# Kernel tuning notes

Hardware: AMD Instinct MI355X
Metric: run time of the kernel (lower is better)

The kernel has to match this reference:

```python
import jax, jax.numpy as jnp
import numpy as np

NUM_GROUPS = 32
EPS = 1e-6


def group_norm(x, gamma, beta):
    # x: (b, c, h, w) -> normalize within 32 groups over (c/g, h, w)
    b, c, h, w = x.shape
    g = NUM_GROUPS
    xg = x.reshape(b, g, c // g, h, w)
    mean = xg.mean(axis=(2, 3, 4), keepdims=True)
    var = xg.var(axis=(2, 3, 4), keepdims=True)
    xg = (xg - mean) * jax.lax.rsqrt(var + EPS)
    xn = xg.reshape(b, c, h, w)
    return xn * gamma[None, :, None, None] + beta[None, :, None, None]


def setup_inputs() -> dict:
    key = jax.random.key(0)
    ks = jax.random.split(key, 4)
    b, c, h, w = 4, 512, 64, 64
    x = jax.random.normal(ks[0], (b, c, h, w), dtype=jnp.float32)
    gamma = jnp.ones((c,), dtype=jnp.float32)
    beta = jnp.zeros((c,), dtype=jnp.float32)
    w_qkv = jax.random.normal(ks[1], (3 * c, c), dtype=jnp.float32) * (1.0 / np.sqrt(c))
    b_qkv = jnp.zeros((3 * c,), dtype=jnp.float32)
    # NOTE: original init zeroes proj weight; use small random weights so the
    # attention path contributes to output/gradients in the baseline.
    w_proj = jax.random.normal(ks[2], (c, c), dtype=jnp.float32) * 0.02
    b_proj = jnp.zeros((c,), dtype=jnp.float32)
    return {"x": x, "gamma": gamma, "beta": beta, "w_qkv": w_qkv,
            "b_qkv": b_qkv, "w_proj": w_proj, "b_proj": b_proj}


def reference(x, gamma, beta, w_qkv, b_qkv, w_proj, b_proj):
    b, c, h, w = x.shape
    scale = c ** (-0.25)
    identity = x
    xn = group_norm(x, gamma, beta)
    # 1x1 conv == channel matmul: (b,c,h,w) x (3c,c) -> (b,3c,h,w)
    qkv = jnp.einsum('bchw,oc->bohw', xn, w_qkv) + b_qkv[None, :, None, None]
    qkv = qkv.reshape(b, 3 * c, h * w)
    q, k, v = jnp.split(qkv, 3, axis=1)          # each (b, c, N)
    attn = jnp.einsum('bci,bcj->bij', q * scale, k * scale)  # (b, N, N)
    attn = jax.nn.softmax(attn, axis=-1)
    out = jnp.einsum('bij,bcj->bci', attn, v)    # (b, c, N)
    out = out.reshape(b, c, h, w)
    out = jnp.einsum('bchw,oc->bohw', out, w_proj) + b_proj[None, :, None, None]
    return out + identity
```

## Files before the change

kernel.cpp:

```cpp
#include <hip/hip_runtime.h>
#include <hip/hip_fp8.h>
#include <stdint.h>

typedef unsigned short u16;
typedef unsigned char u8;
typedef __bf16 bf16x8 __attribute__((ext_vector_type(8)));
typedef float f32x4 __attribute__((ext_vector_type(4)));

__device__ __forceinline__ u16 f2bf(float f) {
  union { float f; unsigned u; } v; v.f = f;
  return (u16)((v.u + 0x7FFFu + ((v.u >> 16) & 1u)) >> 16);
}
__device__ __forceinline__ u8 f2f8(float f) {
  __hip_fp8_e4m3 h(f);
  return (u8)h.__x;
}

__device__ __forceinline__ void gld_lds16(const void* g, void* l) {
  uint32_t lo = (uint32_t)(uintptr_t)l;
  lo = __builtin_amdgcn_readfirstlane(lo);
  auto* lp = (__attribute__((address_space(3))) uint32_t*)(uintptr_t)lo;
  auto* gp = (const __attribute__((address_space(1))) uint32_t*)(uintptr_t)g;
  __builtin_amdgcn_global_load_lds(gp, lp, 16, 0, 0);
}

__device__ __forceinline__ void bar() {
  __builtin_amdgcn_sched_barrier(0);
  __builtin_amdgcn_s_barrier();
  __builtin_amdgcn_sched_barrier(0);
}

__global__ __launch_bounds__(256) void cvt_weights(
    const float* __restrict__ wq, const float* __restrict__ wp,
    u16* __restrict__ oq, u16* __restrict__ op) {
  int i = blockIdx.x * 256 + threadIdx.x;
  if (i < 1536 * 512) oq[i] = f2bf(wq[i]);
  if (i < 512 * 512)  op[i] = f2bf(wp[i]);
}

__global__ __launch_bounds__(256) void gn_stats(const float* __restrict__ x,
                                                float* __restrict__ stats) {
  int bg = blockIdx.x;
  const float* p = x + (size_t)bg * 65536;
  float s = 0.f, sq = 0.f;
  for (int i = threadIdx.x * 4; i < 65536; i += 1024) {
    float4 v = *(const float4*)(p + i);
    s += v.x + v.y + v.z + v.w;
    sq += v.x * v.x + v.y * v.y + v.z * v.z + v.w * v.w;
  }
  int lane = threadIdx.x & 63, w = threadIdx.x >> 6;
  for (int off = 32; off; off >>= 1) {
    s += __shfl_down(s, off);
    sq += __shfl_down(sq, off);
  }
  __shared__ float ls[4], lq[4];
  if (lane == 0) { ls[w] = s; lq[w] = sq; }
  __syncthreads();
  if (threadIdx.x == 0) {
    float S = ls[0] + ls[1] + ls[2] + ls[3];
    float Q = lq[0] + lq[1] + lq[2] + lq[3];
    float mean = S * (1.f / 65536.f);
    float var = Q * (1.f / 65536.f) - mean * mean;
    stats[bg * 2] = mean;
    stats[bg * 2 + 1] = rsqrtf(var + 1e-6f);
  }
}

__global__ __launch_bounds__(256) void gn_norm_t(const float* __restrict__ x,
    const float* __restrict__ stats, const float* __restrict__ gamma,
    const float* __restrict__ beta, u16* __restrict__ xnT) {
  __shared__ u16 tile[64][72];
  int b = blockIdx.z;
  int c0 = blockIdx.y * 64, n0 = blockIdx.x * 64;
  int t = threadIdx.x;
  int cl = t >> 2, ng = (t & 3) * 16;
  int c = c0 + cl;
  float mean = stats[(b * 32 + (c >> 4)) * 2];
  float rstd = stats[(b * 32 + (c >> 4)) * 2 + 1];
  float a = gamma[c] * rstd;
  float b2 = beta[c] - mean * a;
  const float* src = x + ((size_t)b * 512 + c) * 4096 + n0 + ng;
  u16 e[16];
  #pragma unroll
  for (int q = 0; q < 4; ++q) {
    float4 v = *(const float4*)(src + q * 4);
    e[q * 4 + 0] = f2bf(v.x * a + b2);
    e[q * 4 + 1] = f2bf(v.y * a + b2);
    e[q * 4 + 2] = f2bf(v.z * a + b2);
    e[q * 4 + 3] = f2bf(v.w * a + b2);
  }
  #pragma unroll
  for (int j = 0; j < 16; ++j) tile[ng + j][cl] = e[j];
  __syncthreads();
  int nl = t >> 2, cg = (t & 3) * 16;
  uint4 w0 = *(const uint4*)&tile[nl][cg];
  uint4 w1 = *(const uint4*)&tile[nl][cg + 8];
  u16* dst = xnT + ((size_t)b * 4096 + n0 + nl) * 512 + c0 + cg;
  *(uint4*)dst = w0;
  *(uint4*)(dst + 8) = w1;
}

template<int EPI>
__global__ __launch_bounds__(256) void gemm_nt(
    const u16* __restrict__ A, const u16* __restrict__ B,
    int lda, int ldb, int K,
    const float* __restrict__ bias, const float* __restrict__ resid,
    float scale, float* __restrict__ outF, void* __restrict__ outBv, int ldo,
    size_t azs, size_t bzs, size_t ozs) {
  __shared__ __align__(16) u16 smem[16384];
  const size_t z = blockIdx.z;
  A += z * azs; B += z * bzs;
  const int t = threadIdx.x;
  const int wave = t >> 6, lane = t & 63;
  const int wm = wave >> 1, wn = wave & 1;
  const int quad = lane >> 4, li = lane & 15;
  const int m0 = blockIdx.y * 128, n0 = blockIdx.x * 128;

  const int srow = lane >> 2;
  const int scol = (lane & 3) * 8;
  const u16* gA[2];
  const u16* gB[2];
  int ldsOff[2];
  #pragma unroll
  for (int r = 0; r < 2; ++r) {
    int rb = wave + 4 * r;
    gA[r] = A + (size_t)(m0 + rb * 16 + srow) * lda + scol;
    gB[r] = B + (size_t)(n0 + rb * 16 + srow) * ldb + scol;
    ldsOff[r] = rb * 512;
  }

  f32x4 zero = {0.f, 0.f, 0.f, 0.f};
  f32x4 acc[4][4];
  #pragma unroll
  for (int i = 0; i < 4; ++i)
    #pragma unroll
    for (int j = 0; j < 4; ++j) acc[i][j] = zero;

  #pragma unroll
  for (int r = 0; r < 2; ++r) {
    gld_lds16(gA[r], &smem[ldsOff[r]]);
    gld_lds16(gB[r], &smem[8192 + ldsOff[r]]);
  }
  __syncthreads();

  for (int kt = 0; kt < K; kt += 32) {
    const int s = (kt >> 5) & 1;
    if (kt + 32 < K) {
      const int ns = s ^ 1;
      #pragma unroll
      for (int r = 0; r < 2; ++r) {
        gld_lds16(gA[r] + kt + 32, &smem[ns * 4096 + ldsOff[r]]);
        gld_lds16(gB[r] + kt + 32, &smem[8192 + ns * 4096 + ldsOff[r]]);
      }
    }
    bf16x8 af[4], bf[4];
    #pragma unroll
    for (int i = 0; i < 4; ++i) {
      af[i] = *(const bf16x8*)&smem[s * 4096 +
               (wm * 64 + i * 16 + li) * 32 + quad * 8];
      bf[i] = *(const bf16x8*)&smem[8192 + s * 4096 +
               (wn * 64 + i * 16 + li) * 32 + quad * 8];
    }
    #pragma unroll
    for (int i = 0; i < 4; ++i)
      #pragma unroll
      for (int j = 0; j < 4; ++j)
        acc[i][j] = __builtin_amdgcn_mfma_f32_16x16x32_bf16(
            af[i], bf[j], acc[i][j], 0, 0, 0);
    __syncthreads();
  }

  if (EPI == 3) {
    outF += z * ozs; resid += z * ozs;
    #pragma unroll
    for (int i = 0; i < 4; ++i)
      #pragma unroll
      for (int j = 0; j < 4; ++j) {
        int mB = m0 + wm * 64 + i * 16 + quad * 4;
        int n = n0 + wn * 64 + j * 16 + li;
        #pragma unroll
        for (int r = 0; r < 4; ++r) {
          int m = mB + r;
          float v = acc[i][j][r] + bias[m] + resid[(size_t)m * ldo + n];
          outF[(size_t)m * ldo + n] = v;
        }
      }
    return;
  }

  u8* out8 = (u8*)outBv + z * ozs;
  u8* bnc = (u8*)smem;
  #pragma unroll
  for (int i = 0; i < 4; ++i) {
    int lm = wm * 64 + i * 16 + quad * 4;
    #pragma unroll
    for (int j = 0; j < 4; ++j) {
      int ln = wn * 64 + j * 16 + li;
      #pragma unroll
      for (int r = 0; r < 4; ++r) {
        float v = acc[i][j][r];
        u8 o;
        if (EPI == 4) o = f2f8((v + bias[n0 + ln]) * scale);
        else          o = f2f8(v + bias[m0 + lm + r]);
        bnc[(lm + r) * 144 + ln] = o;
      }
    }
  }
  __syncthreads();
  {
    int row = t >> 1, half = t & 1;
    const u8* src = &bnc[row * 144 + half * 64];
    u8* dst = out8 + (size_t)(m0 + row) * ldo + n0 + half * 64;
    #pragma unroll
    for (int cc = 0; cc < 4; ++cc)
      *(uint4*)(dst + cc * 16) = *(const uint4*)(src + cc * 16);
  }
}

template<int EPI, int SWZ>
__global__ __launch_bounds__(256) void gemm_nt8(
    const u8* __restrict__ A, const u8* __restrict__ B,
    int lda, int ldb, int K,
    const float* __restrict__ rsum, float* __restrict__ outF,
    void* __restrict__ outBv, int ldo,
    size_t azs, size_t bzs, size_t ozs) {
  __shared__ __align__(16) u8 smem[49152];
  const size_t z = blockIdx.z;
  A += z * azs; B += z * bzs;
  int bx = blockIdx.x, by = blockIdx.y;
  if (SWZ) {
    int lin = by * 32 + bx;
    int tt = lin >> 8, w = lin & 255;
    by = (tt >> 1) * 16 + (w >> 4);
    bx = (tt & 1) * 16 + (w & 15);
  }
  const int t = threadIdx.x;
  const int wave = t >> 6, lane = t & 63;
  const int wm = wave >> 1, wn = wave & 1;
  const int quad = lane >> 4, li = lane & 15;
  const int m0 = by * 128, n0 = bx * 128;

  const int us = lane ^ ((lane >> 3) & 7);
  const int srow = (us >> 1) & 31;
  const int shalf = us & 1;
  const u8* gA = A + (size_t)(m0 + wave * 32 + srow) * lda + shalf * 16;
  const u8* gB = B + (size_t)(n0 + wave * 32 + srow) * ldb + shalf * 16;
  const int ldsOff = wave * 1024;

  const int h = quad >> 1, qlo = (quad & 1) * 8;
  int aoff[4], boff[4];
  #pragma unroll
  for (int i = 0; i < 4; ++i) {
    int r5 = (i & 1) * 16 + li;
    int p = (2 * r5 + h) ^ ((r5 >> 2) & 7);
    aoff[i] = (wm * 2 + (i >> 1)) * 1024 + p * 16 + qlo;
    boff[i] = (wn * 2 + (i >> 1)) * 1024 + p * 16 + qlo;
  }

  f32x4 zero = {0.f, 0.f, 0.f, 0.f};
  f32x4 acc[4][4];
  #pragma unroll
  for (int i = 0; i < 4; ++i)
    #pragma unroll
    for (int j = 0; j < 4; ++j) acc[i][j] = zero;

  #pragma unroll
  for (int p = 0; p < 2; ++p) {
    gld_lds16(gA + p * 64,      &smem[p * 8192 + ldsOff]);
    gld_lds16(gA + p * 64 + 32, &smem[p * 8192 + 4096 + ldsOff]);
    gld_lds16(gB + p * 64,      &smem[24576 + p * 8192 + ldsOff]);
    gld_lds16(gB + p * 64 + 32, &smem[24576 + p * 8192 + 4096 + ldsOff]);
  }
  __builtin_amdgcn_sched_barrier(0);
  asm volatile("s_waitcnt vmcnt(4)");
  bar();

  int s = 0;
  for (int kt = 0; kt < K; kt += 64) {
    if (kt + 128 < K) {
      const int ns = (s == 0) ? 2 : s - 1;
      gld_lds16(gA + kt + 128,      &smem[ns * 8192 + ldsOff]);
      gld_lds16(gA + kt + 128 + 32, &smem[ns * 8192 + 4096 + ldsOff]);
      gld_lds16(gB + kt + 128,      &smem[24576 + ns * 8192 + ldsOff]);
      gld_lds16(gB + kt + 128 + 32, &smem[24576 + ns * 8192 + 4096 + ldsOff]);
    }
    const int sb = s * 8192;
    long af[4][2], bf[4][2];
    #pragma unroll
    for (int i = 0; i < 4; ++i) {
      #pragma unroll
      for (int g = 0; g < 2; ++g) {
        af[i][g] = *(const long*)&smem[sb + g * 4096 + aoff[i]];
        bf[i][g] = *(const long*)&smem[24576 + sb + g * 4096 + boff[i]];
      }
    }
    #pragma unroll
    for (int i = 0; i < 4; ++i)
      #pragma unroll
      for (int j = 0; j < 4; ++j) {
        acc[i][j] = __builtin_amdgcn_mfma_f32_16x16x32_fp8_fp8(
            af[i][0], bf[j][0], acc[i][j], 0, 0, 0);
        acc[i][j] = __builtin_amdgcn_mfma_f32_16x16x32_fp8_fp8(
            af[i][1], bf[j][1], acc[i][j], 0, 0, 0);
      }
    if (kt + 64 < K) {
      __builtin_amdgcn_sched_barrier(0);
      if (kt + 128 < K) asm volatile("s_waitcnt vmcnt(4)");
      else              asm volatile("s_waitcnt vmcnt(0)");
      bar();
    }
    s = (s == 2) ? 0 : s + 1;
  }
  __syncthreads();

  {
    const float* rsF = rsum + z * 4096;
    u16* outp = (u16*)outBv + z * ozs;
    u16* b16 = (u16*)smem;
    #pragma unroll
    for (int i = 0; i < 4; ++i) {
      int lm = wm * 64 + i * 16 + quad * 4;
      float rinv[4];
      #pragma unroll
      for (int r = 0; r < 4; ++r)
        rinv[r] = __builtin_amdgcn_rcpf(rsF[m0 + lm + r]);
      #pragma unroll
      for (int j = 0; j < 4; ++j) {
        int ln = wn * 64 + j * 16 + li;
        #pragma unroll
        for (int r = 0; r < 4; ++r)
          b16[(lm + r) * 136 + ln] = f2bf(acc[i][j][r] * rinv[r]);
      }
    }
    __syncthreads();
    int row = t >> 1, half = t & 1;
    const u16* src = &b16[row * 136 + half * 64];
    u16* dst = outp + (size_t)(m0 + row) * ldo + n0 + half * 64;
    #pragma unroll
    for (int cc = 0; cc < 8; ++cc)
      *(uint4*)(dst + cc * 8) = *(const uint4*)(src + cc * 8);
  }
}

__global__ __launch_bounds__(256) void qk256(
    const u8* __restrict__ A, const u8* __restrict__ B,
    float* __restrict__ rowsum, u8* __restrict__ outE) {
  __shared__ __align__(16) u8 smem[73728];
  const int lda = 1024, K = 512;
  const size_t z = blockIdx.z;
  A += (size_t)z * 4096 * 1024;
  B += (size_t)z * 4096 * 1024;
  float* rsF = rowsum + (size_t)z * 4096;
  u8* outp = outE + (size_t)z * 4096 * 4096;

  const int t = threadIdx.x;
  const int w = t >> 6, lane = t & 63;
  const int quad = lane >> 4, li = lane & 15;
  const int m0 = blockIdx.y * 256, n0 = blockIdx.x * 128;

  const int us = lane ^ ((lane >> 3) & 7);
  const int srow = (us >> 1) & 31;
  const int shalf = us & 1;
  const u8* gA0 = A + (size_t)(m0 + w * 64 + srow) * lda + shalf * 16;
  const u8* gA1 = gA0 + (size_t)32 * lda;
  const u8* gB  = B + (size_t)(n0 + w * 32 + srow) * lda + shalf * 16;

  const int h = quad >> 1, qlo = (quad & 1) * 8;
  int aoff[4], boff[8];
  #pragma unroll
  for (int i = 0; i < 4; ++i) {
    int r5 = (i & 1) * 16 + li;
    int p = (2 * r5 + h) ^ ((r5 >> 2) & 7);
    aoff[i] = (2 * w + (i >> 1)) * 1024 + p * 16 + qlo;
  }
  #pragma unroll
  for (int j = 0; j < 8; ++j) {
    int r5 = (j & 1) * 16 + li;
    int p = (2 * r5 + h) ^ ((r5 >> 2) & 7);
    boff[j] = (j >> 1) * 1024 + p * 16 + qlo;
  }

  f32x4 zero = {0.f, 0.f, 0.f, 0.f};
  f32x4 acc[4][8];
  #pragma unroll
  for (int i = 0; i < 4; ++i)
    #pragma unroll
    for (int j = 0; j < 8; ++j) acc[i][j] = zero;

  auto STAGE = [&](int kt, int st) {
    int sA = st * 16384, sB = 49152 + st * 8192;
    #pragma unroll
    for (int g = 0; g < 2; ++g) {
      gld_lds16(gA0 + kt + g * 32, &smem[sA + g * 8192 + (2 * w) * 1024]);
      gld_lds16(gA1 + kt + g * 32, &smem[sA + g * 8192 + (2 * w + 1) * 1024]);
      gld_lds16(gB  + kt + g * 32, &smem[sB + g * 4096 + w * 1024]);
    }
  };

  STAGE(0, 0);
  STAGE(64, 1);
  __builtin_amdgcn_sched_barrier(0);
  asm volatile("s_waitcnt vmcnt(6)");
  bar();

  int s = 0;
  for (int kt = 0; kt < K; kt += 64) {
    if (kt + 128 < K) STAGE(kt + 128, (s == 0) ? 2 : s - 1);
    const int sA = s * 16384, sB = 49152 + s * 8192;
    long af[4][2];
    #pragma unroll
    for (int i = 0; i < 4; ++i)
      #pragma unroll
      for (int g = 0; g < 2; ++g)
        af[i][g] = *(const long*)&smem[sA + g * 8192 + aoff[i]];
    #pragma unroll
    for (int j = 0; j < 8; ++j) {
      long b0 = *(const long*)&smem[sB + boff[j]];
      long b1 = *(const long*)&smem[sB + 4096 + boff[j]];
      #pragma unroll
      for (int i = 0; i < 4; ++i) {
        acc[i][j] = __builtin_amdgcn_mfma_f32_16x16x32_fp8_fp8(
            af[i][0], b0, acc[i][j], 0, 0, 0);
        acc[i][j] = __builtin_amdgcn_mfma_f32_16x16x32_fp8_fp8(
            af[i][1], b1, acc[i][j], 0, 0, 0);
      }
    }
    if (kt + 64 < K) {
      __builtin_amdgcn_sched_barrier(0);
      if (kt + 128 < K) asm volatile("s_waitcnt vmcnt(6)");
      else              asm volatile("s_waitcnt vmcnt(0)");
      bar();
    }
    s = (s == 2) ? 0 : s + 1;
  }
  __syncthreads();

  #pragma unroll
  for (int i = 0; i < 4; ++i) {
    int lm = w * 64 + i * 16 + quad * 4;
    float rs[4] = {0.f, 0.f, 0.f, 0.f};
    #pragma unroll
    for (int j = 0; j < 8; ++j) {
      int ln = j * 16 + li;
      #pragma unroll
      for (int r = 0; r < 4; ++r) {
        float e = fminf(__expf(acc[i][j][r]), 448.f);
        smem[(lm + r) * 144 + ln] = f2f8(e);
        rs[r] += e;
      }
    }
    #pragma unroll
    for (int r = 0; r < 4; ++r) {
      rs[r] += __shfl_xor(rs[r], 1);
      rs[r] += __shfl_xor(rs[r], 2);
      rs[r] += __shfl_xor(rs[r], 4);
      rs[r] += __shfl_xor(rs[r], 8);
    }
    if (li == 0) {
      #pragma unroll
      for (int r = 0; r < 4; ++r) atomicAdd(&rsF[m0 + lm + r], rs[r]);
    }
  }
  __syncthreads();
  {
    int row = t;
    const u8* src = &smem[row * 144];
    u8* dst = outp + (size_t)(m0 + row) * 4096 + n0;
    #pragma unroll
    for (int cc = 0; cc < 8; ++cc)
      *(uint4*)(dst + cc * 16) = *(const uint4*)(src + cc * 16);
  }
}

extern "C" void kernel_launch(void* const* d_in, const int* in_sizes, int n_in,
                              void* d_out, int out_size, void* d_ws, size_t ws_size,
                              hipStream_t stream) {
  (void)in_sizes; (void)n_in; (void)out_size; (void)ws_size;
  const float* x      = (const float*)d_in[0];
  const float* gamma  = (const float*)d_in[1];
  const float* beta   = (const float*)d_in[2];
  const float* w_qkv  = (const float*)d_in[3];
  const float* b_qkv  = (const float*)d_in[4];
  const float* w_proj = (const float*)d_in[5];
  const float* b_proj = (const float*)d_in[6];
  float* out = (float*)d_out;

  const int C = 512, N = 4096;
  const size_t NC = (size_t)N * C;
  const float scale = 0.21022410381342863f;

  char* ws = (char*)d_ws;
  size_t off = 0;
  auto alloc = [&](size_t bytes) -> char* {
    char* p = ws + off; off += (bytes + 255) & ~(size_t)255; return p;
  };
  u16*   wq_bf  = (u16*)alloc((size_t)1536 * 512 * 2);
  u16*   wp_bf  = (u16*)alloc((size_t)512 * 512 * 2);
  float* stats  = (float*)alloc(128 * 2 * 4);
  float* rowsum = (float*)alloc((size_t)4 * N * 4);
  u16*   xnT    = (u16*)alloc((size_t)4 * NC * 2);
  u8*    qkT    = (u8*)alloc((size_t)4 * N * 1024);
  u8*    vbf    = (u8*)alloc((size_t)4 * 512 * 4096);
  u16*   ao     = (u16*)alloc((size_t)4 * NC * 2);
  u8*    E      = (u8*)alloc((size_t)4 * N * N);

  cvt_weights<<<3072, 256, 0, stream>>>(w_qkv, w_proj, wq_bf, wp_bf);
  gn_stats<<<128, 256, 0, stream>>>(x, stats);
  gn_norm_t<<<dim3(64, 8, 4), 256, 0, stream>>>(x, stats, gamma, beta, xnT);
  hipMemsetAsync(rowsum, 0, (size_t)4 * N * 4, stream);

  gemm_nt<4><<<dim3(8, 32, 4), 256, 0, stream>>>(
      xnT, wq_bf, 512, 512, 512, b_qkv, nullptr, scale,
      nullptr, qkT, 1024, NC, 0, (size_t)N * 1024);
  gemm_nt<5><<<dim3(32, 4, 4), 256, 0, stream>>>(
      wq_bf + (size_t)1024 * 512, xnT, 512, 512, 512, b_qkv + 1024, nullptr,
      0.f, nullptr, vbf, 4096, 0, NC, (size_t)512 * 4096);
  qk256<<<dim3(32, 16, 4), 256, 0, stream>>>(qkT, qkT + 512, rowsum, E);
  gemm_nt8<6, 0><<<dim3(4, 32, 4), 256, 0, stream>>>(
      E, vbf, 4096, 4096, 4096, rowsum, nullptr,
      ao, 512, (size_t)N * N, (size_t)512 * 4096, NC);
  gemm_nt<3><<<dim3(32, 4, 4), 256, 0, stream>>>(
      wp_bf, ao, 512, 512, 512, b_proj, x, 0.f,
      out, nullptr, 4096, 0, NC, NC);
}
```

Baseline: 393.1 us.

## Restructure QK kernel into persistent strips over eight column tiles

Replaces the per-tile QK^T exp kernel (256x128 tiles, one block per tile) with a strip kernel where each block owns 128 rows and walks 1024 columns in eight 128-wide tiles. A single continuous three-stage K pipeline runs across tile boundaries. Row sums accumulate in registers, so each row needs only one atomicAdd per strip. The aim is to cut block launch and prologue overhead, pipeline bubbles and atomic traffic. The cost is a smaller per-tile MFMA footprint with more A reloads, plus extra barriers for the mid-loop exp/store epilogue.

```diff
diff --git a/kernel.cpp b/kernel.cpp
--- a/kernel.cpp
+++ b/kernel.cpp
@@ -342,11 +342,11 @@
   }
 }
 
-__global__ __launch_bounds__(256) void qk256(
+__global__ __launch_bounds__(256) void qk_strip(
     const u8* __restrict__ A, const u8* __restrict__ B,
     float* __restrict__ rowsum, u8* __restrict__ outE) {
-  __shared__ __align__(16) u8 smem[73728];
-  const int lda = 1024, K = 512;
+  __shared__ __align__(16) u8 smem[67584];
+  const int lda = 1024;
   const size_t z = blockIdx.z;
   A += (size_t)z * 4096 * 1024;
   B += (size_t)z * 4096 * 1024;
@@ -354,121 +354,137 @@
   u8* outp = outE + (size_t)z * 4096 * 4096;
 
   const int t = threadIdx.x;
-  const int w = t >> 6, lane = t & 63;
+  const int wave = t >> 6, lane = t & 63;
+  const int wm = wave >> 1, wn = wave & 1;
   const int quad = lane >> 4, li = lane & 15;
-  const int m0 = blockIdx.y * 256, n0 = blockIdx.x * 128;
+  const int m0 = blockIdx.y * 128;
+  const int nbase = blockIdx.x * 1024;
 
   const int us = lane ^ ((lane >> 3) & 7);
   const int srow = (us >> 1) & 31;
   const int shalf = us & 1;
-  const u8* gA0 = A + (size_t)(m0 + w * 64 + srow) * lda + shalf * 16;
-  const u8* gA1 = gA0 + (size_t)32 * lda;
-  const u8* gB  = B + (size_t)(n0 + w * 32 + srow) * lda + shalf * 16;
+  const u8* gA = A + (size_t)(m0 + wave * 32 + srow) * lda + shalf * 16;
+  const u8* gBb = B + (size_t)(nbase + wave * 32 + srow) * lda + shalf * 16;
+  const int ldsOff = wave * 1024;
 
   const int h = quad >> 1, qlo = (quad & 1) * 8;
-  int aoff[4], boff[8];
+  int aoff[4], boff[4];
   #pragma unroll
   for (int i = 0; i < 4; ++i) {
     int r5 = (i & 1) * 16 + li;
     int p = (2 * r5 + h) ^ ((r5 >> 2) & 7);
-    aoff[i] = (2 * w + (i >> 1)) * 1024 + p * 16 + qlo;
-  }
-  #pragma unroll
-  for (int j = 0; j < 8; ++j) {
-    int r5 = (j & 1) * 16 + li;
-    int p = (2 * r5 + h) ^ ((r5 >> 2) & 7);
-    boff[j] = (j >> 1) * 1024 + p * 16 + qlo;
+    aoff[i] = (wm * 2 + (i >> 1)) * 1024 + p * 16 + qlo;
+    boff[i] = (wn * 2 + (i >> 1)) * 1024 + p * 16 + qlo;
   }
 
   f32x4 zero = {0.f, 0.f, 0.f, 0.f};
-  f32x4 acc[4][8];
+  f32x4 acc[4][4];
   #pragma unroll
   for (int i = 0; i < 4; ++i)
     #pragma unroll
-    for (int j = 0; j < 8; ++j) acc[i][j] = zero;
-
-  auto STAGE = [&](int kt, int st) {
-    int sA = st * 16384, sB = 49152 + st * 8192;
-    #pragma unroll
-    for (int g = 0; g < 2; ++g) {
-      gld_lds16(gA0 + kt + g * 32, &smem[sA + g * 8192 + (2 * w) * 1024]);
-      gld_lds16(gA1 + kt + g * 32, &smem[sA + g * 8192 + (2 * w + 1) * 1024]);
-      gld_lds16(gB  + kt + g * 32, &smem[sB + g * 4096 + w * 1024]);
-    }
+    for (int j = 0; j < 4; ++j) acc[i][j] = zero;
+  float rs_tot[4][4];
+  #pragma unroll
+  for (int i = 0; i < 4; ++i)
+    #pragma unroll
+    for (int r = 0; r < 4; ++r) rs_tot[i][r] = 0.f;
+
+  auto STAGE = [&](int v, int st) {
+    int nt = v >> 3, kt = (v & 7) * 64;
+    const u8* ga = gA + kt;
+    const u8* gb = gBb + (size_t)(nt * 128) * 1024 + kt;
+    gld_lds16(ga,      &smem[st * 8192 + ldsOff]);
+    gld_lds16(ga + 32, &smem[st * 8192 + 4096 + ldsOff]);
+    gld_lds16(gb,      &smem[24576 + st * 8192 + ldsOff]);
+    gld_lds16(gb + 32, &smem[24576 + st * 8192 + 4096 + ldsOff]);
   };
 
   STAGE(0, 0);
-  STAGE(64, 1);
+  STAGE(1, 1);
   __builtin_amdgcn_sched_barrier(0);
-  asm volatile("s_waitcnt vmcnt(6)");
+  asm volatile("s_waitcnt vmcnt(4)");
   bar();
 
   int s = 0;
-  for (int kt = 0; kt < K; kt += 64) {
-    if (kt + 128 < K) STAGE(kt + 128, (s == 0) ? 2 : s - 1);
-    const int sA = s * 16384, sB = 49152 + s * 8192;
-    long af[4][2];
+  #pragma unroll 1
+  for (int v = 0; v < 64; ++v) {
+    if (v + 2 < 64) STAGE(v + 2, (s == 0) ? 2 : s - 1);
+    const int sb = s * 8192;
+    long af[4][2], bf[4][2];
+    #pragma unroll
+    for (int i = 0; i < 4; ++i) {
+      #pragma unroll
+      for (int g = 0; g < 2; ++g) {
+        af[i][g] = *(const long*)&smem[sb + g * 4096 + aoff[i]];
+        bf[i][g] = *(const long*)&smem[24576 + sb + g * 4096 + boff[i]];
+      }
+    }
     #pragma unroll
     for (int i = 0; i < 4; ++i)
       #pragma unroll
-      for (int g = 0; g < 2; ++g)
-        af[i][g] = *(const long*)&smem[sA + g * 8192 + aoff[i]];
-    #pragma unroll
-    for (int j = 0; j < 8; ++j) {
-      long b0 = *(const long*)&smem[sB + boff[j]];
-      long b1 = *(const long*)&smem[sB + 4096 + boff[j]];
+      for (int j = 0; j < 4; ++j) {
+        acc[i][j] = __builtin_amdgcn_mfma_f32_16x16x32_fp8_fp8(
+            af[i][0], bf[j][0], acc[i][j], 0, 0, 0);
+        acc[i][j] = __builtin_amdgcn_mfma_f32_16x16x32_fp8_fp8(
+            af[i][1], bf[j][1], acc[i][j], 0, 0, 0);
+      }
+
+    if ((v & 7) == 7) {
+      int n0e = nbase + (v >> 3) * 128;
+      bar();
       #pragma unroll
       for (int i = 0; i < 4; ++i) {
-        acc[i][j] = __builtin_amdgcn_mfma_f32_16x16x32_fp8_fp8(
-            af[i][0], b0, acc[i][j], 0, 0, 0);
-        acc[i][j] = __builtin_amdgcn_mfma_f32_16x16x32_fp8_fp8(
-            af[i][1], b1, acc[i][j], 0, 0, 0);
-      }
-    }
-    if (kt + 64 < K) {
+        int lm = wm * 64 + i * 16 + quad * 4;
+        #pragma unroll
+        for (int j = 0; j < 4; ++j) {
+          int ln = wn * 64 + j * 16 + li;
+          #pragma unroll
+          for (int r = 0; r < 4; ++r) {
+            float e = fminf(__expf(acc[i][j][r]), 448.f);
+            smem[49152 + (lm + r) * 144 + ln] = f2f8(e);
+            rs_tot[i][r] += e;
+          }
+          acc[i][j] = zero;
+        }
+      }
       __builtin_amdgcn_sched_barrier(0);
-      if (kt + 128 < K) asm volatile("s_waitcnt vmcnt(6)");
-      else              asm volatile("s_waitcnt vmcnt(0)");
+      asm volatile("s_waitcnt lgkmcnt(0)");
       bar();
+      {
+        int row = t >> 1, half = t & 1;
+        const u8* src = &smem[49152 + row * 144 + half * 64];
+        u8* dst = outp + (size_t)(m0 + row) * 4096 + n0e + half * 64;
+        #pragma unroll
+        for (int cc = 0; cc < 4; ++cc)
+          *(uint4*)(dst + cc * 16) = *(const uint4*)(src + cc * 16);
+      }
+      bar();
+      if (v + 1 < 64) {
+        __builtin_amdgcn_sched_barrier(0);
+        asm volatile("s_waitcnt vmcnt(8)");
+        bar();
+      }
+    } else {
+      __builtin_amdgcn_sched_barrier(0);
+      if (v + 2 < 64) asm volatile("s_waitcnt vmcnt(4)");
+      else            asm volatile("s_waitcnt vmcnt(0)");
+      bar();
     }
     s = (s == 2) ? 0 : s + 1;
   }
-  __syncthreads();
 
   #pragma unroll
   for (int i = 0; i < 4; ++i) {
-    int lm = w * 64 + i * 16 + quad * 4;
-    float rs[4] = {0.f, 0.f, 0.f, 0.f};
-    #pragma unroll
-    for (int j = 0; j < 8; ++j) {
-      int ln = j * 16 + li;
-      #pragma unroll
-      for (int r = 0; r < 4; ++r) {
-        float e = fminf(__expf(acc[i][j][r]), 448.f);
-        smem[(lm + r) * 144 + ln] = f2f8(e);
-        rs[r] += e;
-      }
-    }
+    int lm = wm * 64 + i * 16 + quad * 4;
     #pragma unroll
     for (int r = 0; r < 4; ++r) {
-      rs[r] += __shfl_xor(rs[r], 1);
-      rs[r] += __shfl_xor(rs[r], 2);
-      rs[r] += __shfl_xor(rs[r], 4);
-      rs[r] += __shfl_xor(rs[r], 8);
-    }
-    if (li == 0) {
-      #pragma unroll
-      for (int r = 0; r < 4; ++r) atomicAdd(&rsF[m0 + lm + r], rs[r]);
-    }
-  }
-  __syncthreads();
-  {
-    int row = t;
-    const u8* src = &smem[row * 144];
-    u8* dst = outp + (size_t)(m0 + row) * 4096 + n0;
-    #pragma unroll
-    for (int cc = 0; cc < 8; ++cc)
-      *(uint4*)(dst + cc * 16) = *(const uint4*)(src + cc * 16);
+      float rv = rs_tot[i][r];
+      rv += __shfl_xor(rv, 1);
+      rv += __shfl_xor(rv, 2);
+      rv += __shfl_xor(rv, 4);
+      rv += __shfl_xor(rv, 8);
+      if (li == 0) atomicAdd(&rsF[m0 + lm + r], rv);
+    }
   }
 }
 
@@ -515,7 +531,7 @@
   gemm_nt<5><<<dim3(32, 4, 4), 256, 0, stream>>>(
       wq_bf + (size_t)1024 * 512, xnT, 512, 512, 512, b_qkv + 1024, nullptr,
       0.f, nullptr, vbf, 4096, 0, NC, (size_t)512 * 4096);
-  qk256<<<dim3(32, 16, 4), 256, 0, stream>>>(qkT, qkT + 512, rowsum, E);
+  qk_strip<<<dim3(4, 32, 4), 256, 0, stream>>>(qkT, qkT + 512, rowsum, E);
   gemm_nt8<6, 0><<<dim3(4, 32, 4), 256, 0, stream>>>(
       E, vbf, 4096, 4096, 4096, rowsum, nullptr,
       ao, 512, (size_t)N * N, (size_t)512 * 4096, NC);
```

After: 378.8 us. 3.6% less time.

## Split QK^T exp kernel tile across 8 waves instead of 4

Applied to the files above, without the earlier changes.

The fp8 QK^T + exp kernel now launches 512 threads (8 waves) per 256x128 block, arranged 4x2, so each wave computes a 64x64 sub-tile instead of 64x128. This halves per-wave accumulator registers and B-fragment loads and adds more waves for latency hiding. Only half the waves load B tiles, so the vmcnt waits are made wave-dependent. The cost is more LDS reads of A fragments overall and possibly lower occupancy given 72KB of LDS per block.

```diff
diff --git a/kernel.cpp b/kernel.cpp
--- a/kernel.cpp
+++ b/kernel.cpp
@@ -342,7 +342,7 @@
   }
 }
 
-__global__ __launch_bounds__(256) void qk256(
+__global__ __launch_bounds__(512, 4) void qk8w(
     const u8* __restrict__ A, const u8* __restrict__ B,
     float* __restrict__ rowsum, u8* __restrict__ outE) {
   __shared__ __align__(16) u8 smem[73728];
@@ -355,80 +355,81 @@
 
   const int t = threadIdx.x;
   const int w = t >> 6, lane = t & 63;
+  const int wm = w >> 1, wn = w & 1;
   const int quad = lane >> 4, li = lane & 15;
   const int m0 = blockIdx.y * 256, n0 = blockIdx.x * 128;
 
   const int us = lane ^ ((lane >> 3) & 7);
   const int srow = (us >> 1) & 31;
   const int shalf = us & 1;
-  const u8* gA0 = A + (size_t)(m0 + w * 64 + srow) * lda + shalf * 16;
-  const u8* gA1 = gA0 + (size_t)32 * lda;
-  const u8* gB  = B + (size_t)(n0 + w * 32 + srow) * lda + shalf * 16;
+  const u8* gA = A + (size_t)(m0 + w * 32 + srow) * lda + shalf * 16;
+  const bool doB = w < 4;
+  const u8* gB = B + (size_t)(n0 + (w & 3) * 32 + srow) * lda + shalf * 16;
 
   const int h = quad >> 1, qlo = (quad & 1) * 8;
-  int aoff[4], boff[8];
+  int aoff[4], boff[4];
   #pragma unroll
   for (int i = 0; i < 4; ++i) {
     int r5 = (i & 1) * 16 + li;
     int p = (2 * r5 + h) ^ ((r5 >> 2) & 7);
-    aoff[i] = (2 * w + (i >> 1)) * 1024 + p * 16 + qlo;
-  }
-  #pragma unroll
-  for (int j = 0; j < 8; ++j) {
-    int r5 = (j & 1) * 16 + li;
-    int p = (2 * r5 + h) ^ ((r5 >> 2) & 7);
-    boff[j] = (j >> 1) * 1024 + p * 16 + qlo;
+    aoff[i] = (wm * 2 + (i >> 1)) * 1024 + p * 16 + qlo;
+    boff[i] = (wn * 2 + (i >> 1)) * 1024 + p * 16 + qlo;
   }
 
   f32x4 zero = {0.f, 0.f, 0.f, 0.f};
-  f32x4 acc[4][8];
+  f32x4 acc[4][4];
   #pragma unroll
   for (int i = 0; i < 4; ++i)
     #pragma unroll
-    for (int j = 0; j < 8; ++j) acc[i][j] = zero;
+    for (int j = 0; j < 4; ++j) acc[i][j] = zero;
 
   auto STAGE = [&](int kt, int st) {
     int sA = st * 16384, sB = 49152 + st * 8192;
     #pragma unroll
     for (int g = 0; g < 2; ++g) {
-      gld_lds16(gA0 + kt + g * 32, &smem[sA + g * 8192 + (2 * w) * 1024]);
-      gld_lds16(gA1 + kt + g * 32, &smem[sA + g * 8192 + (2 * w + 1) * 1024]);
-      gld_lds16(gB  + kt + g * 32, &smem[sB + g * 4096 + w * 1024]);
+      gld_lds16(gA + kt + g * 32, &smem[sA + g * 8192 + w * 1024]);
+      if (doB)
+        gld_lds16(gB + kt + g * 32, &smem[sB + g * 4096 + (w & 3) * 1024]);
     }
   };
 
   STAGE(0, 0);
   STAGE(64, 1);
   __builtin_amdgcn_sched_barrier(0);
-  asm volatile("s_waitcnt vmcnt(6)");
+  if (doB) asm volatile("s_waitcnt vmcnt(4)");
+  else     asm volatile("s_waitcnt vmcnt(2)");
   bar();
 
   int s = 0;
   for (int kt = 0; kt < K; kt += 64) {
     if (kt + 128 < K) STAGE(kt + 128, (s == 0) ? 2 : s - 1);
     const int sA = s * 16384, sB = 49152 + s * 8192;
-    long af[4][2];
+    long af[4][2], bf[4][2];
+    #pragma unroll
+    for (int i = 0; i < 4; ++i) {
+      #pragma unroll
+      for (int g = 0; g < 2; ++g) {
+        af[i][g] = *(const long*)&smem[sA + g * 8192 + aoff[i]];
+        bf[i][g] = *(const long*)&smem[sB + g * 4096 + boff[i]];
+      }
+    }
     #pragma unroll
     for (int i = 0; i < 4; ++i)
       #pragma unroll
-      for (int g = 0; g < 2; ++g)
-        af[i][g] = *(const long*)&smem[sA + g * 8192 + aoff[i]];
-    #pragma unroll
-    for (int j = 0; j < 8; ++j) {
-      long b0 = *(const long*)&smem[sB + boff[j]];
-      long b1 = *(const long*)&smem[sB + 4096 + boff[j]];
-      #pragma unroll
-      for (int i = 0; i < 4; ++i) {
+      for (int j = 0; j < 4; ++j) {
         acc[i][j] = __builtin_amdgcn_mfma_f32_16x16x32_fp8_fp8(
-            af[i][0], b0, acc[i][j], 0, 0, 0);
+            af[i][0], bf[j][0], acc[i][j], 0, 0, 0);
         acc[i][j] = __builtin_amdgcn_mfma_f32_16x16x32_fp8_fp8(
-            af[i][1], b1, acc[i][j], 0, 0, 0);
-      }
-    }
+            af[i][1], bf[j][1], acc[i][j], 0, 0, 0);
+      }
     if (kt + 64 < K) {
       __builtin_amdgcn_sched_barrier(0);
-      if (kt + 128 < K) asm volatile("s_waitcnt vmcnt(6)");
-      else              asm volatile("s_waitcnt vmcnt(0)");
+      if (kt + 128 < K) {
+        if (doB) asm volatile("s_waitcnt vmcnt(4)");
+        else     asm volatile("s_waitcnt vmcnt(2)");
+      } else {
+        asm volatile("s_waitcnt vmcnt(0)");
+      }
       bar();
     }
     s = (s == 2) ? 0 : s + 1;
@@ -437,11 +438,11 @@
 
   #pragma unroll
   for (int i = 0; i < 4; ++i) {
-    int lm = w * 64 + i * 16 + quad * 4;
+    int lm = wm * 64 + i * 16 + quad * 4;
     float rs[4] = {0.f, 0.f, 0.f, 0.f};
     #pragma unroll
-    for (int j = 0; j < 8; ++j) {
-      int ln = j * 16 + li;
+    for (int j = 0; j < 4; ++j) {
+      int ln = wn * 64 + j * 16 + li;
       #pragma unroll
       for (int r = 0; r < 4; ++r) {
         float e = fminf(__expf(acc[i][j][r]), 448.f);
@@ -463,11 +464,11 @@
   }
   __syncthreads();
   {
-    int row = t;
-    const u8* src = &smem[row * 144];
-    u8* dst = outp + (size_t)(m0 + row) * 4096 + n0;
-    #pragma unroll
-    for (int cc = 0; cc < 8; ++cc)
+    int row = t >> 1, half = t & 1;
+    const u8* src = &smem[row * 144 + half * 64];
+    u8* dst = outp + (size_t)(m0 + row) * 4096 + n0 + half * 64;
+    #pragma unroll
+    for (int cc = 0; cc < 4; ++cc)
       *(uint4*)(dst + cc * 16) = *(const uint4*)(src + cc * 16);
   }
 }
@@ -515,7 +516,7 @@
   gemm_nt<5><<<dim3(32, 4, 4), 256, 0, stream>>>(
       wq_bf + (size_t)1024 * 512, xnT, 512, 512, 512, b_qkv + 1024, nullptr,
       0.f, nullptr, vbf, 4096, 0, NC, (size_t)512 * 4096);
-  qk256<<<dim3(32, 16, 4), 256, 0, stream>>>(qkT, qkT + 512, rowsum, E);
+  qk8w<<<dim3(32, 16, 4), 512, 0, stream>>>(qkT, qkT + 512, rowsum, E);
   gemm_nt8<6, 0><<<dim3(4, 32, 4), 256, 0, stream>>>(
       E, vbf, 4096, 4096, 4096, rowsum, nullptr,
       ao, 512, (size_t)N * N, (size_t)512 * 4096, NC);
```

New measurement: 366.2 us. 6.9% less time.
